# Optimization experiments

Hardware: AMD Instinct MI355X
Metric: run time of the kernel (lower is better)

## Reference

```python
import jax, jax.numpy as jnp
import numpy as np

N_USERS = 100001
N_ITEMS = 200001
EMBED_DIM = 64
N_LAYERS = 3
NNZ = 3_200_000  # unique user-item interactions (before dedup)


def setup_inputs() -> dict:
    key = jax.random.key(0)
    rng = np.random.default_rng(0)
    # random bipartite interactions, deduped (dok_matrix dict semantics)
    u = rng.integers(0, N_USERS, NNZ).astype(np.int64)
    it = rng.integers(0, N_ITEMS, NNZ).astype(np.int64)
    pair = np.unique(u * N_ITEMS + it)
    u = pair // N_ITEMS
    it = pair % N_ITEMS
    N = N_USERS + N_ITEMS
    # symmetric adjacency edges: user->item and item->user blocks
    row = np.concatenate([u, it + N_USERS])
    col = np.concatenate([it + N_USERS, u])
    # L = D^-1/2 A D^-1/2 with degree from binary A, eps=1e-7 as in source
    deg = np.bincount(row, minlength=N).astype(np.float32) + 1e-7
    dinv = deg ** -0.5
    vals = (dinv[row] * dinv[col]).astype(np.float32)
    k1, k2 = jax.random.split(key)
    user_emb = jax.random.normal(k1, (N_USERS, EMBED_DIM), jnp.float32) * 0.1
    item_emb = jax.random.normal(k2, (N_ITEMS, EMBED_DIM), jnp.float32) * 0.1
    return {
        "user_emb": user_emb,
        "item_emb": item_emb,
        "row": jnp.asarray(row),
        "col": jnp.asarray(col),
        "vals": jnp.asarray(vals),
        "n_layers": N_LAYERS,
        "n_users": N_USERS,
    }


def reference(user_emb, item_emb, row, col, vals, n_layers, n_users):
    N = user_emb.shape[0] + item_emb.shape[0]
    x = jnp.concatenate([user_emb, item_emb], axis=0)  # [N, D] ego embeddings
    acc = x  # running sum fuses stack+mean over layers
    for _ in range(n_layers):
        # SpMM: out[r] += vals[e] * x[col[e]] for each edge e with row[e]=r
        x = jax.ops.segment_sum(vals[:, None] * x[col], row, num_segments=N)
        acc = acc + x
    out = acc / (n_layers + 1)  # mean over (n_layers+1) layer outputs
    return out[:n_users], out[n_users:]
```

## Files before the change

### kernel.cpp

```cpp
#include <hip/hip_runtime.h>

#define TPB 256
#define NWG 256
#define KB_BITS 8
#define MAXB 12288

__device__ __forceinline__ unsigned int bf16pair(float a, float b) {
  unsigned int ua = __float_as_uint(a);
  ua += 0x7fffu + ((ua >> 16) & 1u);
  unsigned int ub = __float_as_uint(b);
  ub += 0x7fffu + ((ub >> 16) & 1u);
  return (ua >> 16) | (ub & 0xffff0000u);
}
__device__ __forceinline__ float bf16lo(unsigned int u) { return __uint_as_float(u << 16); }
__device__ __forceinline__ float bf16hi(unsigned int u) { return __uint_as_float(u & 0xffff0000u); }

typedef unsigned int u32x4v __attribute__((ext_vector_type(4)));
typedef float f32x4v __attribute__((ext_vector_type(4)));

__device__ __forceinline__ uint4 ntload_u4(const uint4* p) {
  u32x4v v = __builtin_nontemporal_load(reinterpret_cast<const u32x4v*>(p));
  return make_uint4(v.x, v.y, v.z, v.w);
}
__device__ __forceinline__ float4 ntload_f4(const float4* p) {
  f32x4v v = __builtin_nontemporal_load(reinterpret_cast<const f32x4v*>(p));
  return make_float4(v.x, v.y, v.z, v.w);
}
__device__ __forceinline__ void ntstore_u4(uint4* p, uint4 v) {
  u32x4v t; t.x = v.x; t.y = v.y; t.z = v.z; t.w = v.w;
  __builtin_nontemporal_store(t, reinterpret_cast<u32x4v*>(p));
}
__device__ __forceinline__ void ntstore_f4(float4* p, float4 v) {
  f32x4v t; t.x = v.x; t.y = v.y; t.z = v.z; t.w = v.w;
  __builtin_nontemporal_store(t, reinterpret_cast<f32x4v*>(p));
}

__global__ void rp_user_and_hist(const int* __restrict__ row, int* __restrict__ rp,
                                 int* __restrict__ wgcnt,
                                 int Eh, int E, int NU, int K, int chunk, int BU) {
  extern __shared__ int hist[];
  if ((int)blockIdx.x < BU) {
    int e = blockIdx.x * TPB + threadIdx.x;
    if (e >= Eh) return;
    int r = row[e];
    int rprev = (e == 0) ? -1 : row[e - 1];
    for (int rr = rprev + 1; rr <= r; ++rr) rp[rr] = e;
    if (e == Eh - 1) {
      for (int rr = r + 1; rr < NU; ++rr) rp[rr] = Eh;
    }
  } else {
    int w = blockIdx.x - BU, tid = threadIdx.x;
    for (int b = tid; b < K; b += TPB) hist[b] = 0;
    __syncthreads();
    int s = Eh + w * chunk;
    int e_end = s + chunk; if (e_end > E) e_end = E;
    for (int e = s + tid; e < e_end; e += TPB)
      atomicAdd(&hist[(row[e] - NU) >> KB_BITS], 1);
    __syncthreads();
    for (int b = tid; b < K; b += TPB) wgcnt[b * NWG + w] = hist[b];
  }
}

__global__ void p2a_scan(int* __restrict__ wgcnt, int* __restrict__ btot) {
  __shared__ int sc[TPB];
  int b = blockIdx.x, t = threadIdx.x;
  int v = wgcnt[b * NWG + t];
  sc[t] = v; __syncthreads();
  for (int off = 1; off < TPB; off <<= 1) {
    int x = (t >= off) ? sc[t - off] : 0;
    __syncthreads(); sc[t] += x; __syncthreads();
  }
  wgcnt[b * NWG + t] = sc[t] - v;
  if (t == 0) btot[b] = sc[TPB - 1];
}

__global__ void p2b_scan(const int* __restrict__ btot, int* __restrict__ rpB,
                         int* __restrict__ rp, int K, int Eh, int E, int NU, int NI) {
  __shared__ int sc[TPB];
  __shared__ int carry;
  int t = threadIdx.x;
  if (t == 0) carry = Eh;
  __syncthreads();
  for (int base = 0; base < K; base += TPB) {
    int idx = base + t;
    int v = (idx < K) ? btot[idx] : 0;
    sc[t] = v; __syncthreads();
    for (int off = 1; off < TPB; off <<= 1) {
      int x = (t >= off) ? sc[t - off] : 0;
      __syncthreads(); sc[t] += x; __syncthreads();
    }
    int c = carry;
    if (idx < K) rpB[idx] = c + sc[t] - v;
    __syncthreads();
    if (t == 0) carry = c + sc[TPB - 1];
    __syncthreads();
  }
  if (t == 0) { rpB[K] = E; rp[NU + NI] = E; }
}

__global__ void p3_part(const int* __restrict__ row, const int* __restrict__ col,
                        const int* __restrict__ wgcnt, const int* __restrict__ rpB,
                        unsigned int* __restrict__ evcol,
                        int Eh, int E, int NU, int K, int chunk) {
  extern __shared__ int pos[];
  int w = blockIdx.x, tid = threadIdx.x;
  for (int b = tid; b < K; b += TPB) pos[b] = rpB[b] + wgcnt[b * NWG + w];
  __syncthreads();
  int s = Eh + w * chunk;
  int e_end = s + chunk; if (e_end > E) e_end = E;
  for (int e = s + tid; e < e_end; e += TPB) {
    int li = row[e] - NU;
    int b = li >> KB_BITS;
    int p = atomicAdd(&pos[b], 1);
    evcol[p] = ((unsigned int)(li & 255) << 24) | (unsigned int)col[e];
  }
}

__global__ void p4_sort(unsigned int* __restrict__ evcol, const int* __restrict__ rpB,
                        int* __restrict__ rp, int NU, int NI) {
  __shared__ unsigned int lcol[MAXB];
  __shared__ int bins[256], sc[TPB];
  int b = blockIdx.x, t = threadIdx.x;
  int start = rpB[b], end = rpB[b + 1];
  int nb = end - start;
  for (int i = t; i < nb; i += TPB) lcol[i] = evcol[start + i];
  bins[t] = 0;
  __syncthreads();
  for (int i = t; i < nb; i += TPB) atomicAdd(&bins[lcol[i] >> 24], 1);
  __syncthreads();
  int v = bins[t];
  sc[t] = v; __syncthreads();
  for (int off = 1; off < TPB; off <<= 1) {
    int x = (t >= off) ? sc[t - off] : 0;
    __syncthreads(); sc[t] += x; __syncthreads();
  }
  int excl = sc[t] - v;
  int item = (b << KB_BITS) + t;
  if (item < NI) rp[NU + item] = start + excl;
  bins[t] = excl;
  __syncthreads();
  for (int i = t; i < nb; i += TPB) {
    unsigned int pk = lcol[i];
    int p = atomicAdd(&bins[pk >> 24], 1);
    evcol[start + p] = pk & 0xFFFFFFu;
  }
}

__global__ void init_scaled(const float* __restrict__ u, const float* __restrict__ it,
                            const int* __restrict__ rp,
                            uint2* __restrict__ x0, int NU16, int N16) {
  int i = blockIdx.x * TPB + threadIdx.x;
  if (i >= N16) return;
  float4 v = (i < NU16) ? ntload_f4(reinterpret_cast<const float4*>(u) + i)
                        : ntload_f4(reinterpret_cast<const float4*>(it) + (i - NU16));
  int r = i >> 4;
  float deg = (float)(rp[r + 1] - rp[r]) + 1e-7f;
  float dv = rsqrtf(deg);
  x0[i] = make_uint2(bf16pair(dv * v.x, dv * v.y), bf16pair(dv * v.z, dv * v.w));
}

__device__ __forceinline__ void gather_row(const uint4* __restrict__ xv4,
                                           const unsigned int* __restrict__ ec,
                                           int start, int end, int l, float* a) {
#pragma unroll
  for (int k = 0; k < 8; ++k) a[k] = 0.f;
  int j = start;
  for (; j + 3 < end; j += 4) {
    unsigned int c0 = ec[j], c1 = ec[j + 1], c2 = ec[j + 2], c3 = ec[j + 3];
    uint4 p0 = xv4[(size_t)c0 * 8 + l];
    uint4 p1 = xv4[(size_t)c1 * 8 + l];
    uint4 p2 = xv4[(size_t)c2 * 8 + l];
    uint4 p3 = xv4[(size_t)c3 * 8 + l];
    a[0] += bf16lo(p0.x); a[1] += bf16hi(p0.x); a[2] += bf16lo(p0.y); a[3] += bf16hi(p0.y);
    a[4] += bf16lo(p0.z); a[5] += bf16hi(p0.z); a[6] += bf16lo(p0.w); a[7] += bf16hi(p0.w);
    a[0] += bf16lo(p1.x); a[1] += bf16hi(p1.x); a[2] += bf16lo(p1.y); a[3] += bf16hi(p1.y);
    a[4] += bf16lo(p1.z); a[5] += bf16hi(p1.z); a[6] += bf16lo(p1.w); a[7] += bf16hi(p1.w);
    a[0] += bf16lo(p2.x); a[1] += bf16hi(p2.x); a[2] += bf16lo(p2.y); a[3] += bf16hi(p2.y);
    a[4] += bf16lo(p2.z); a[5] += bf16hi(p2.z); a[6] += bf16lo(p2.w); a[7] += bf16hi(p2.w);
    a[0] += bf16lo(p3.x); a[1] += bf16hi(p3.x); a[2] += bf16lo(p3.y); a[3] += bf16hi(p3.y);
    a[4] += bf16lo(p3.z); a[5] += bf16hi(p3.z); a[6] += bf16lo(p3.w); a[7] += bf16hi(p3.w);
  }
  for (; j < end; ++j) {
    unsigned int c0 = ec[j];
    uint4 p = xv4[(size_t)c0 * 8 + l];
    a[0] += bf16lo(p.x); a[1] += bf16hi(p.x); a[2] += bf16lo(p.y); a[3] += bf16hi(p.y);
    a[4] += bf16lo(p.z); a[5] += bf16hi(p.z); a[6] += bf16lo(p.w); a[7] += bf16hi(p.w);
  }
}

__global__ void spmm_kernel(const unsigned int* __restrict__ x, unsigned int* __restrict__ y,
                            const int* __restrict__ rp,
                            const unsigned int* __restrict__ col_u,
                            const unsigned int* __restrict__ evcol, int N, int NU) {
  int t = blockIdx.x * TPB + threadIdx.x;
  int g = t >> 3;
  int l = t & 7;
  if (g >= N) return;
  int start = rp[g], end = rp[g + 1];
  const unsigned int* ec = (g < NU) ? col_u : evcol;
  float a[8];
  gather_row(reinterpret_cast<const uint4*>(x), ec, start, end, l, a);
  float d2 = 1.0f / ((float)(end - start) + 1e-7f);
  uint4 yo;
  yo.x = bf16pair(d2 * a[0], d2 * a[1]); yo.y = bf16pair(d2 * a[2], d2 * a[3]);
  yo.z = bf16pair(d2 * a[4], d2 * a[5]); yo.w = bf16pair(d2 * a[6], d2 * a[7]);
  ntstore_u4(reinterpret_cast<uint4*>(y) + (size_t)g * 8 + l, yo);
}

__global__ void spmm_last_kernel(const unsigned int* __restrict__ x,
                                 const int* __restrict__ rp,
                                 const unsigned int* __restrict__ col_u,
                                 const unsigned int* __restrict__ evcol,
                                 const unsigned int* __restrict__ x1,
                                 const unsigned int* __restrict__ x2,
                                 const float* __restrict__ uemb,
                                 const float* __restrict__ iemb,
                                 float* __restrict__ out, int N, int NU) {
  int t = blockIdx.x * TPB + threadIdx.x;
  int g = t >> 3;
  int l = t & 7;
  if (g >= N) return;
  int start = rp[g], end = rp[g + 1];
  const unsigned int* ec = (g < NU) ? col_u : evcol;
  float a[8];
  gather_row(reinterpret_cast<const uint4*>(x), ec, start, end, l, a);
  float deg = (float)(end - start) + 1e-7f;
  float dinv = rsqrtf(deg);
  float sq = deg * dinv;
  uint4 p1 = ntload_u4(reinterpret_cast<const uint4*>(x1) + (size_t)g * 8 + l);
  uint4 p2 = reinterpret_cast<const uint4*>(x2)[(size_t)g * 8 + l];
  const float4* ep = (g < NU)
      ? reinterpret_cast<const float4*>(uemb) + (size_t)g * 16
      : reinterpret_cast<const float4*>(iemb) + (size_t)(g - NU) * 16;
  float4 e0 = ntload_f4(ep + 2 * l), e1 = ntload_f4(ep + 2 * l + 1);
  float t0 = bf16lo(p1.x) + bf16lo(p2.x), t1 = bf16hi(p1.x) + bf16hi(p2.x);
  float t2 = bf16lo(p1.y) + bf16lo(p2.y), t3 = bf16hi(p1.y) + bf16hi(p2.y);
  float t4 = bf16lo(p1.z) + bf16lo(p2.z), t5 = bf16hi(p1.z) + bf16hi(p2.z);
  float t6 = bf16lo(p1.w) + bf16lo(p2.w), t7 = bf16hi(p1.w) + bf16hi(p2.w);
  float4 o0, o1;
  o0.x = 0.25f * (e0.x + sq * t0 + dinv * a[0]);
  o0.y = 0.25f * (e0.y + sq * t1 + dinv * a[1]);
  o0.z = 0.25f * (e0.z + sq * t2 + dinv * a[2]);
  o0.w = 0.25f * (e0.w + sq * t3 + dinv * a[3]);
  o1.x = 0.25f * (e1.x + sq * t4 + dinv * a[4]);
  o1.y = 0.25f * (e1.y + sq * t5 + dinv * a[5]);
  o1.z = 0.25f * (e1.z + sq * t6 + dinv * a[6]);
  o1.w = 0.25f * (e1.w + sq * t7 + dinv * a[7]);
  float4* op = reinterpret_cast<float4*>(out) + (size_t)g * 16;
  ntstore_f4(op + 2 * l, o0);
  ntstore_f4(op + 2 * l + 1, o1);
}

static inline char* align256(char* p) {
  return (char*)(((uintptr_t)p + 255) & ~(uintptr_t)255);
}

extern "C" void kernel_launch(void* const* d_in, const int* in_sizes, int n_in,
                              void* d_out, int out_size, void* d_ws, size_t ws_size,
                              hipStream_t stream) {
  const float* user_emb = (const float*)d_in[0];
  const float* item_emb = (const float*)d_in[1];
  const int* row = (const int*)d_in[2];
  const int* col = (const int*)d_in[3];

  const int NU = in_sizes[0] / 64;
  const int NI = in_sizes[1] / 64;
  const int N = NU + NI;
  const int E = in_sizes[2];
  const int Eh = E / 2;
  const int Eh2 = E - Eh;

  float* out = (float*)d_out;

  const int K = (NI + 255) >> KB_BITS;

  char* p = (char*)d_ws;
  unsigned int* xb[3];
  for (int k = 0; k < 3; ++k) { xb[k] = (unsigned int*)p; p = align256(p + (size_t)N * 64 * 2); }
  int* rp = (int*)p;                   p = align256(p + (size_t)(N + 1) * 4);
  int* wgcnt = (int*)p;                p = align256(p + (size_t)K * NWG * 4);
  int* btot = (int*)p;                 p = align256(p + (size_t)K * 4);
  int* rpB = (int*)p;                  p = align256(p + (size_t)(K + 1) * 4);
  unsigned int* evcol = (unsigned int*)p;

  const int N16 = N * 16;
  const int NU16 = NU * 16;
  const int chunk = (Eh2 + NWG - 1) / NWG;
  const int BU = (Eh + TPB - 1) / TPB;

  rp_user_and_hist<<<BU + NWG, TPB, K * 4, stream>>>(row, rp, wgcnt, Eh, E, NU, K, chunk, BU);
  p2a_scan<<<K, TPB, 0, stream>>>(wgcnt, btot);
  p2b_scan<<<1, TPB, 0, stream>>>(btot, rpB, rp, K, Eh, E, NU, NI);
  p3_part<<<NWG, TPB, K * 4, stream>>>(row, col, wgcnt, rpB, evcol, Eh, E, NU, K, chunk);
  p4_sort<<<K, TPB, 0, stream>>>(evcol, rpB, rp, NU, NI);

  init_scaled<<<(N16 + TPB - 1) / TPB, TPB, 0, stream>>>(user_emb, item_emb, rp,
                                                         (uint2*)xb[0], NU16, N16);

  const int spmm_blocks = (N * 8 + TPB - 1) / TPB;
  spmm_kernel<<<spmm_blocks, TPB, 0, stream>>>(xb[0], xb[1], rp,
                                               (const unsigned int*)col, evcol, N, NU);
  spmm_kernel<<<spmm_blocks, TPB, 0, stream>>>(xb[1], xb[2], rp,
                                               (const unsigned int*)col, evcol, N, NU);
  spmm_last_kernel<<<spmm_blocks, TPB, 0, stream>>>(xb[2], rp,
                                                    (const unsigned int*)col, evcol,
                                                    xb[1], xb[2], user_emb, item_emb,
                                                    out, N, NU);
}
```

Before: 631.2 us.

## Build item CSR with global atomic degree count and cursor scatter

Replaces the two-level bucket partition and in-LDS sort for the item-side CSR with a direct per-item degree histogram using global atomics, a scan over it, and a scatter that claims slots through a per-item cursor. This removes the per-workgroup bucket count matrix, the partition pass and the local sort kernel. In exchange it relies on global atomics across about 200k counters. Edge order within each item row becomes nondeterministic, so float summation order can vary from run to run.

```diff
diff --git a/kernel.cpp b/kernel.cpp
--- a/kernel.cpp
+++ b/kernel.cpp
@@ -2,8 +2,8 @@
 
 #define TPB 256
 #define NWG 256
+#define IBLK 256
 #define KB_BITS 8
-#define MAXB 12288
 
 __device__ __forceinline__ unsigned int bf16pair(float a, float b) {
   unsigned int ua = __float_as_uint(a);
@@ -35,10 +35,9 @@
   __builtin_nontemporal_store(t, reinterpret_cast<f32x4v*>(p));
 }
 
-__global__ void rp_user_and_hist(const int* __restrict__ row, int* __restrict__ rp,
-                                 int* __restrict__ wgcnt,
-                                 int Eh, int E, int NU, int K, int chunk, int BU) {
-  extern __shared__ int hist[];
+__global__ void k1_rp_hist(const int* __restrict__ row, int* __restrict__ rp,
+                           int* __restrict__ ideg,
+                           int Eh, int E, int NU, int BU) {
   if ((int)blockIdx.x < BU) {
     int e = blockIdx.x * TPB + threadIdx.x;
     if (e >= Eh) return;
@@ -49,100 +48,68 @@
       for (int rr = r + 1; rr < NU; ++rr) rp[rr] = Eh;
     }
   } else {
-    int w = blockIdx.x - BU, tid = threadIdx.x;
-    for (int b = tid; b < K; b += TPB) hist[b] = 0;
-    __syncthreads();
-    int s = Eh + w * chunk;
-    int e_end = s + chunk; if (e_end > E) e_end = E;
-    for (int e = s + tid; e < e_end; e += TPB)
-      atomicAdd(&hist[(row[e] - NU) >> KB_BITS], 1);
-    __syncthreads();
-    for (int b = tid; b < K; b += TPB) wgcnt[b * NWG + w] = hist[b];
-  }
-}
-
-__global__ void p2a_scan(int* __restrict__ wgcnt, int* __restrict__ btot) {
+    int w = blockIdx.x - BU;
+    for (int e = Eh + w * TPB + threadIdx.x; e < E; e += IBLK * TPB)
+      atomicAdd(&ideg[row[e] - NU], 1);
+  }
+}
+
+__global__ void k2a_scan(int* __restrict__ ideg, int* __restrict__ btot, int NI) {
   __shared__ int sc[TPB];
   int b = blockIdx.x, t = threadIdx.x;
-  int v = wgcnt[b * NWG + t];
+  int idx = b * TPB + t;
+  int v = (idx < NI) ? ideg[idx] : 0;
   sc[t] = v; __syncthreads();
   for (int off = 1; off < TPB; off <<= 1) {
     int x = (t >= off) ? sc[t - off] : 0;
     __syncthreads(); sc[t] += x; __syncthreads();
   }
-  wgcnt[b * NWG + t] = sc[t] - v;
+  if (idx < NI) ideg[idx] = sc[t] - v;
   if (t == 0) btot[b] = sc[TPB - 1];
 }
 
-__global__ void p2b_scan(const int* __restrict__ btot, int* __restrict__ rpB,
-                         int* __restrict__ rp, int K, int Eh, int E, int NU, int NI) {
+__global__ void k2b_scan(const int* __restrict__ btot, int* __restrict__ rpB,
+                         int* __restrict__ rp, int KB, int Eh, int E, int N) {
   __shared__ int sc[TPB];
   __shared__ int carry;
   int t = threadIdx.x;
   if (t == 0) carry = Eh;
   __syncthreads();
-  for (int base = 0; base < K; base += TPB) {
+  for (int base = 0; base < KB; base += TPB) {
     int idx = base + t;
-    int v = (idx < K) ? btot[idx] : 0;
+    int v = (idx < KB) ? btot[idx] : 0;
     sc[t] = v; __syncthreads();
     for (int off = 1; off < TPB; off <<= 1) {
       int x = (t >= off) ? sc[t - off] : 0;
       __syncthreads(); sc[t] += x; __syncthreads();
     }
     int c = carry;
-    if (idx < K) rpB[idx] = c + sc[t] - v;
+    if (idx < KB) rpB[idx] = c + sc[t] - v;
     __syncthreads();
     if (t == 0) carry = c + sc[TPB - 1];
     __syncthreads();
   }
-  if (t == 0) { rpB[K] = E; rp[NU + NI] = E; }
-}
-
-__global__ void p3_part(const int* __restrict__ row, const int* __restrict__ col,
-                        const int* __restrict__ wgcnt, const int* __restrict__ rpB,
-                        unsigned int* __restrict__ evcol,
-                        int Eh, int E, int NU, int K, int chunk) {
-  extern __shared__ int pos[];
-  int w = blockIdx.x, tid = threadIdx.x;
-  for (int b = tid; b < K; b += TPB) pos[b] = rpB[b] + wgcnt[b * NWG + w];
-  __syncthreads();
-  int s = Eh + w * chunk;
-  int e_end = s + chunk; if (e_end > E) e_end = E;
-  for (int e = s + tid; e < e_end; e += TPB) {
-    int li = row[e] - NU;
-    int b = li >> KB_BITS;
-    int p = atomicAdd(&pos[b], 1);
-    evcol[p] = ((unsigned int)(li & 255) << 24) | (unsigned int)col[e];
-  }
-}
-
-__global__ void p4_sort(unsigned int* __restrict__ evcol, const int* __restrict__ rpB,
-                        int* __restrict__ rp, int NU, int NI) {
-  __shared__ unsigned int lcol[MAXB];
-  __shared__ int bins[256], sc[TPB];
-  int b = blockIdx.x, t = threadIdx.x;
-  int start = rpB[b], end = rpB[b + 1];
-  int nb = end - start;
-  for (int i = t; i < nb; i += TPB) lcol[i] = evcol[start + i];
-  bins[t] = 0;
-  __syncthreads();
-  for (int i = t; i < nb; i += TPB) atomicAdd(&bins[lcol[i] >> 24], 1);
-  __syncthreads();
-  int v = bins[t];
-  sc[t] = v; __syncthreads();
-  for (int off = 1; off < TPB; off <<= 1) {
-    int x = (t >= off) ? sc[t - off] : 0;
-    __syncthreads(); sc[t] += x; __syncthreads();
-  }
-  int excl = sc[t] - v;
-  int item = (b << KB_BITS) + t;
-  if (item < NI) rp[NU + item] = start + excl;
-  bins[t] = excl;
-  __syncthreads();
-  for (int i = t; i < nb; i += TPB) {
-    unsigned int pk = lcol[i];
-    int p = atomicAdd(&bins[pk >> 24], 1);
-    evcol[start + p] = pk & 0xFFFFFFu;
+  if (t == 0) { rpB[KB] = E; rp[N] = E; }
+}
+
+__global__ void k2c_fin(const int* __restrict__ ideg, const int* __restrict__ rpB,
+                        int* __restrict__ rp, int* __restrict__ cursor,
+                        int NU, int NI) {
+  int idx = blockIdx.x * TPB + threadIdx.x;
+  if (idx >= NI) return;
+  int v = rpB[blockIdx.x] + ideg[idx];
+  rp[NU + idx] = v;
+  cursor[idx] = v;
+}
+
+__global__ void s1_scatter(const int* __restrict__ row, const int* __restrict__ col,
+                           int* __restrict__ cursor, unsigned int* __restrict__ evcol,
+                           int Eh, int E, int NU) {
+  int w = blockIdx.x;
+  for (int e = Eh + w * TPB + threadIdx.x; e < E; e += NWG * TPB) {
+    int it = row[e] - NU;
+    int slot = atomicAdd(&cursor[it], 1);
+    evcol[slot] = (unsigned int)col[e];
   }
 }
 
@@ -268,31 +235,31 @@
   const int N = NU + NI;
   const int E = in_sizes[2];
   const int Eh = E / 2;
-  const int Eh2 = E - Eh;
 
   float* out = (float*)d_out;
 
-  const int K = (NI + 255) >> KB_BITS;
+  const int KB = (NI + 255) >> KB_BITS;
 
   char* p = (char*)d_ws;
   unsigned int* xb[3];
   for (int k = 0; k < 3; ++k) { xb[k] = (unsigned int*)p; p = align256(p + (size_t)N * 64 * 2); }
   int* rp = (int*)p;                   p = align256(p + (size_t)(N + 1) * 4);
-  int* wgcnt = (int*)p;                p = align256(p + (size_t)K * NWG * 4);
-  int* btot = (int*)p;                 p = align256(p + (size_t)K * 4);
-  int* rpB = (int*)p;                  p = align256(p + (size_t)(K + 1) * 4);
+  int* ideg = (int*)p;                 p = align256(p + (size_t)NI * 4);
+  int* cursor = (int*)p;               p = align256(p + (size_t)NI * 4);
+  int* btot = (int*)p;                 p = align256(p + (size_t)KB * 4);
+  int* rpB = (int*)p;                  p = align256(p + (size_t)(KB + 1) * 4);
   unsigned int* evcol = (unsigned int*)p;
 
   const int N16 = N * 16;
   const int NU16 = NU * 16;
-  const int chunk = (Eh2 + NWG - 1) / NWG;
   const int BU = (Eh + TPB - 1) / TPB;
 
-  rp_user_and_hist<<<BU + NWG, TPB, K * 4, stream>>>(row, rp, wgcnt, Eh, E, NU, K, chunk, BU);
-  p2a_scan<<<K, TPB, 0, stream>>>(wgcnt, btot);
-  p2b_scan<<<1, TPB, 0, stream>>>(btot, rpB, rp, K, Eh, E, NU, NI);
-  p3_part<<<NWG, TPB, K * 4, stream>>>(row, col, wgcnt, rpB, evcol, Eh, E, NU, K, chunk);
-  p4_sort<<<K, TPB, 0, stream>>>(evcol, rpB, rp, NU, NI);
+  hipMemsetAsync(ideg, 0, (size_t)NI * 4, stream);
+  k1_rp_hist<<<BU + IBLK, TPB, 0, stream>>>(row, rp, ideg, Eh, E, NU, BU);
+  k2a_scan<<<KB, TPB, 0, stream>>>(ideg, btot, NI);
+  k2b_scan<<<1, TPB, 0, stream>>>(btot, rpB, rp, KB, Eh, E, N);
+  k2c_fin<<<KB, TPB, 0, stream>>>(ideg, rpB, rp, cursor, NU, NI);
+  s1_scatter<<<NWG, TPB, 0, stream>>>(row, col, cursor, evcol, Eh, E, NU);
 
   init_scaled<<<(N16 + TPB - 1) / TPB, TPB, 0, stream>>>(user_emb, item_emb, rp,
                                                          (uint2*)xb[0], NU16, N16);
```

Result: slower. 873.7 us (+38.4%).
